# Kernel tuning notes

Measured on AMD Instinct MI355X. Metric: run time of the kernel, lower is better.

## Reference

```python
import jax, jax.numpy as jnp
import numpy as np

M, OUT, IN = 16384, 2048, 2048

def setup_inputs() -> dict:
    key = jax.random.key(0)
    k1, k2 = jax.random.split(key)
    x = jax.random.normal(k1, (M, IN), dtype=jnp.float32)
    weight = jax.random.normal(k2, (OUT, IN), dtype=jnp.float32)  # nn.Linear weight [out, in]
    alpha = jnp.ones((1,), dtype=jnp.float32) * 0.5
    return {"x": x, "weight": weight, "alpha": alpha}

def reference(x, weight, alpha):
    # DualRateAlphaFunction forward: binarize weight to sign(w) and scale by learned alpha.
    binary_weight = jnp.sign(weight) * alpha  # [out, in]
    # F.linear(x, binary_weight): x @ binary_weight.T
    return jnp.einsum('mi,oi->mo', x, binary_weight)
```

## Files before the change

### kernel.cpp

```cpp
#include <hip/hip_runtime.h>
#include <stdint.h>
#include <type_traits>

#define M_DIM 16384
#define N_DIM 2048
#define K_DIM 2048

typedef __bf16 bf16_t;
typedef __bf16 bf16x8 __attribute__((ext_vector_type(8)));
typedef __bf16 bf16x4 __attribute__((ext_vector_type(4)));
typedef float f32x4 __attribute__((ext_vector_type(4)));
typedef float f32x16 __attribute__((ext_vector_type(16)));

template <int N> using ic = std::integral_constant<int, N>;

__device__ __forceinline__ void gload_lds16(const void* g, void* l) {
  __builtin_amdgcn_global_load_lds(
      (const __attribute__((address_space(1))) void*)g,
      (__attribute__((address_space(3))) void*)l, 16, 0, 0);
}

template <bool SIGN>
__global__ void cvt_kernel(const float* __restrict__ in, bf16_t* __restrict__ out) {
  long long i = ((long long)blockIdx.x * 256 + threadIdx.x) * 8;
  const float4* p = (const float4*)(in + i);
  float4 v0 = p[0];
  float4 v1 = p[1];
  float f[8] = {v0.x, v0.y, v0.z, v0.w, v1.x, v1.y, v1.z, v1.w};
  bf16x8 r;
#pragma unroll
  for (int j = 0; j < 8; ++j) {
    float v = f[j];
    if (SIGN) v = (v > 0.f) ? 1.f : ((v < 0.f) ? -1.f : 0.f);
    r[j] = (bf16_t)v;
  }
  *(bf16x8*)(out + i) = r;
}

__global__ __launch_bounds__(512, 2) void gemm32(const bf16_t* __restrict__ A,
                                                 const bf16_t* __restrict__ B,
                                                 const float* __restrict__ alpha_p,
                                                 float* __restrict__ C) {
  extern __shared__ char smem[];
  char* AsB = smem;
  char* BsB = smem + 65536;

  const int tid = threadIdx.x;
  const int lane = tid & 63;
  const int wid = tid >> 6;
  const int wm = wid >> 2;
  const int wn = wid & 3;

  const int bid = blockIdx.x;
  const int swz = (bid & 7) * 64 + (bid >> 3);
  const int bm = swz >> 3;
  const int bn = swz & 7;

  const int rl = lane & 31;
  const int kh = lane >> 5;

  const char* apc[4][2];
  const char* bpc[2][2];
#pragma unroll
  for (int mt = 0; mt < 4; ++mt)
#pragma unroll
    for (int k2 = 0; k2 < 2; ++k2) {
      int row = wm * 128 + mt * 32 + rl;
      int c2 = k2 * 32 + kh * 16;
      apc[mt][k2] = AsB + row * 64 + (c2 ^ (((row >> 1) & 3) << 4));
    }
#pragma unroll
  for (int nt = 0; nt < 2; ++nt)
#pragma unroll
    for (int k2 = 0; k2 < 2; ++k2) {
      int row = wn * 64 + nt * 32 + rl;
      int c2 = k2 * 32 + kh * 16;
      bpc[nt][k2] = BsB + row * 64 + (c2 ^ (((row >> 1) & 3) << 4));
    }

  const char* asrc[2];
  const char* bsrc[2];
  char* aldst[2];
  char* bldst[2];
#pragma unroll
  for (int q = 0; q < 2; ++q) {
    int P = q * 8192 + tid * 16;
    int row = P >> 6;
    int lcol = (P & 63) ^ (((row >> 1) & 3) << 4);
    asrc[q] = (const char*)(A + (size_t)(bm * 256 + row) * K_DIM) + lcol;
    bsrc[q] = (const char*)(B + (size_t)(bn * 256 + row) * K_DIM) + lcol;
    aldst[q] = AsB + q * 8192 + wid * 1024;
    bldst[q] = BsB + q * 8192 + wid * 1024;
  }

  f32x16 acc[4][2];
#pragma unroll
  for (int mt = 0; mt < 4; ++mt)
#pragma unroll
    for (int nt = 0; nt < 2; ++nt)
#pragma unroll
      for (int r = 0; r < 16; ++r) acc[mt][nt][r] = 0.f;

#pragma unroll
  for (int tt = 0; tt < 3; ++tt) {
    gload_lds16(asrc[0] + tt * 64, aldst[0] + tt * 16384);
    gload_lds16(asrc[1] + tt * 64, aldst[1] + tt * 16384);
    gload_lds16(bsrc[0] + tt * 64, bldst[0] + tt * 16384);
    gload_lds16(bsrc[1] + tt * 64, bldst[1] + tt * 16384);
  }
  asm volatile("s_waitcnt vmcnt(8)" ::: "memory");
  __builtin_amdgcn_s_barrier();

  auto kstep = [&](auto UC, auto MC) {
    constexpr int U = UC.value;
    constexpr int MODE = MC.value;
    constexpr int SLOT = U * 16384;
    constexpr int PSLOT = ((U + 3) & 3) * 16384;
    constexpr int GOFF = (U + 3) * 64;

    bf16x8 a01[2][2], b[2][2];
#pragma unroll
    for (int mt = 0; mt < 2; ++mt)
#pragma unroll
      for (int k2 = 0; k2 < 2; ++k2)
        a01[mt][k2] = *(const bf16x8*)(apc[mt][k2] + SLOT);
#pragma unroll
    for (int nt = 0; nt < 2; ++nt)
#pragma unroll
      for (int k2 = 0; k2 < 2; ++k2)
        b[nt][k2] = *(const bf16x8*)(bpc[nt][k2] + SLOT);
    if constexpr (MODE == 0) {
      gload_lds16(asrc[0] + GOFF, aldst[0] + PSLOT);
      gload_lds16(asrc[1] + GOFF, aldst[1] + PSLOT);
    }
    __builtin_amdgcn_s_barrier();
    asm volatile("s_waitcnt lgkmcnt(0)" ::: "memory");
    __builtin_amdgcn_s_setprio(1);
#pragma unroll
    for (int k2 = 0; k2 < 2; ++k2)
#pragma unroll
      for (int mt = 0; mt < 2; ++mt)
#pragma unroll
        for (int nt = 0; nt < 2; ++nt)
          acc[mt][nt] = __builtin_amdgcn_mfma_f32_32x32x16_bf16(
              a01[mt][k2], b[nt][k2], acc[mt][nt], 0, 0, 0);
    __builtin_amdgcn_s_setprio(0);
    __builtin_amdgcn_s_barrier();

    bf16x8 a23[2][2];
#pragma unroll
    for (int mt = 0; mt < 2; ++mt)
#pragma unroll
      for (int k2 = 0; k2 < 2; ++k2)
        a23[mt][k2] = *(const bf16x8*)(apc[2 + mt][k2] + SLOT);
    if constexpr (MODE == 0) {
      gload_lds16(bsrc[0] + GOFF, bldst[0] + PSLOT);
      gload_lds16(bsrc[1] + GOFF, bldst[1] + PSLOT);
      asm volatile("s_waitcnt vmcnt(8)" ::: "memory");
    } else if constexpr (MODE == 1) {
      asm volatile("s_waitcnt vmcnt(4)" ::: "memory");
    } else {
      asm volatile("s_waitcnt vmcnt(0)" ::: "memory");
    }
    __builtin_amdgcn_s_barrier();
    asm volatile("s_waitcnt lgkmcnt(0)" ::: "memory");
    __builtin_amdgcn_s_setprio(1);
#pragma unroll
    for (int k2 = 0; k2 < 2; ++k2)
#pragma unroll
      for (int mt = 0; mt < 2; ++mt)
#pragma unroll
        for (int nt = 0; nt < 2; ++nt)
          acc[2 + mt][nt] = __builtin_amdgcn_mfma_f32_32x32x16_bf16(
              a23[mt][k2], b[nt][k2], acc[2 + mt][nt], 0, 0, 0);
    __builtin_amdgcn_s_setprio(0);
    __builtin_amdgcn_s_barrier();
  };

#pragma unroll 1
  for (int T = 0; T < 15; ++T) {
    kstep(ic<0>{}, ic<0>{});
    kstep(ic<1>{}, ic<0>{});
    kstep(ic<2>{}, ic<0>{});
    kstep(ic<3>{}, ic<0>{});
    asrc[0] += 256; asrc[1] += 256; bsrc[0] += 256; bsrc[1] += 256;
  }
  kstep(ic<0>{}, ic<0>{});
  kstep(ic<1>{}, ic<1>{});
  kstep(ic<2>{}, ic<2>{});
  kstep(ic<3>{}, ic<2>{});

  const float alpha = alpha_p[0];
  const int rbase = bm * 256 + wm * 128;
  const int cbase = bn * 256 + wn * 64 + rl;
#pragma unroll
  for (int mt = 0; mt < 4; ++mt)
#pragma unroll
    for (int nt = 0; nt < 2; ++nt)
#pragma unroll
      for (int r = 0; r < 16; ++r) {
        int rr = (r & 3) + 8 * (r >> 2) + 4 * kh;
        C[(size_t)(rbase + mt * 32 + rr) * N_DIM + cbase + nt * 32] =
            alpha * acc[mt][nt][r];
      }
}

__global__ __launch_bounds__(256) void gemm_fallback(const float* __restrict__ Ap,
                                                     const float* __restrict__ Bp,
                                                     const float* __restrict__ alpha_p,
                                                     float* __restrict__ C) {
  __shared__ bf16_t Asf[128 * 32];
  __shared__ bf16_t Bsf[128 * 32];
  const int tid = threadIdx.x;
  const int lane = tid & 63;
  const int wid = tid >> 6;
  const int wr = wid >> 1;
  const int wc = wid & 1;
  const int cpx = gridDim.x >> 3;
  const int bid = blockIdx.x;
  const int swz = (bid & 7) * cpx + (bid >> 3);
  const int NB = N_DIM / 128;
  const int bm = swz / NB;
  const int bn = swz % NB;
  f32x4 acc[4][4];
#pragma unroll
  for (int m = 0; m < 4; ++m)
#pragma unroll
    for (int n = 0; n < 4; ++n) acc[m][n] = (f32x4){0.f, 0.f, 0.f, 0.f};
  const int r0 = lane & 15;
  const int ko = (lane >> 4) * 8;
  for (int kk = 0; kk < K_DIM; kk += 32) {
    const float* Af = Ap + (size_t)bm * 128 * K_DIM + kk;
    const float* Bf = Bp + (size_t)bn * 128 * K_DIM + kk;
#pragma unroll
    for (int q = 0; q < 4; ++q) {
      int e = q * 256 + tid;
      int row = e >> 3;
      int kc = (e & 7) << 2;
      float4 v = *(const float4*)(Af + (size_t)row * K_DIM + kc);
      bf16x4 tv;
      tv[0] = (bf16_t)v.x; tv[1] = (bf16_t)v.y; tv[2] = (bf16_t)v.z; tv[3] = (bf16_t)v.w;
      *(bf16x4*)&Asf[e * 4] = tv;
    }
#pragma unroll
    for (int q = 0; q < 4; ++q) {
      int e = q * 256 + tid;
      int row = e >> 3;
      int kc = (e & 7) << 2;
      float4 v = *(const float4*)(Bf + (size_t)row * K_DIM + kc);
      float s[4] = {v.x, v.y, v.z, v.w};
      bf16x4 tv;
#pragma unroll
      for (int j = 0; j < 4; ++j)
        tv[j] = (bf16_t)((s[j] > 0.f) ? 1.f : ((s[j] < 0.f) ? -1.f : 0.f));
      *(bf16x4*)&Bsf[e * 4] = tv;
    }
    __syncthreads();
    bf16x8 a[4], b[4];
#pragma unroll
    for (int m = 0; m < 4; ++m) a[m] = *(const bf16x8*)&Asf[(wr * 64 + m * 16 + r0) * 32 + ko];
#pragma unroll
    for (int n = 0; n < 4; ++n) b[n] = *(const bf16x8*)&Bsf[(wc * 64 + n * 16 + r0) * 32 + ko];
#pragma unroll
    for (int m = 0; m < 4; ++m)
#pragma unroll
      for (int n = 0; n < 4; ++n)
        acc[m][n] = __builtin_amdgcn_mfma_f32_16x16x32_bf16(a[m], b[n], acc[m][n], 0, 0, 0);
    __syncthreads();
  }
  const float alpha = alpha_p[0];
  const int rowb = bm * 128 + wr * 64 + (lane >> 4) * 4;
  const int colb = bn * 128 + wc * 64 + r0;
#pragma unroll
  for (int m = 0; m < 4; ++m)
#pragma unroll
    for (int n = 0; n < 4; ++n)
#pragma unroll
      for (int r = 0; r < 4; ++r)
        C[(size_t)(rowb + m * 16 + r) * N_DIM + colb + n * 16] = alpha * acc[m][n][r];
}

extern "C" void kernel_launch(void* const* d_in, const int* in_sizes, int n_in,
                              void* d_out, int out_size, void* d_ws, size_t ws_size,
                              hipStream_t stream) {
  const float* x = (const float*)d_in[0];
  const float* w = (const float*)d_in[1];
  const float* alpha = (const float*)d_in[2];
  float* out = (float*)d_out;

  const size_t nx = (size_t)M_DIM * K_DIM;
  const size_t nw = (size_t)N_DIM * K_DIM;
  const size_t need = (nx + nw) * sizeof(bf16_t);

  if (ws_size >= need) {
    bf16_t* xb = (bf16_t*)d_ws;
    bf16_t* wb = xb + nx;
    cvt_kernel<false><<<(int)(nx / 2048), 256, 0, stream>>>(x, xb);
    cvt_kernel<true><<<(int)(nw / 2048), 256, 0, stream>>>(w, wb);
    (void)hipFuncSetAttribute((const void*)gemm32,
                              hipFuncAttributeMaxDynamicSharedMemorySize, 131072);
    gemm32<<<512, 512, 131072, stream>>>(xb, wb, alpha, out);
  } else {
    gemm_fallback<<<(M_DIM / 128) * (N_DIM / 128), 256, 0, stream>>>(x, w, alpha, out);
  }
}
```

Measured before the change: 172.3 us.

## Prefetch next-slot LDS fragments across k-steps and re-layout LDS in 16-row subblocks

Restructures the GEMM main loop so the A01 and B fragments for the next k-slot are read from LDS during the current step, using double-buffered B registers. This removes one barrier and an lgkmcnt(0) wait per half-step and issues all four global-to-LDS prefetches together. It also changes the LDS tile layout to 16-row subblocks with a new XOR swizzle, aiming to cut bank conflicts on the fragment reads. In exchange it holds more VGPRs for the register double-buffering and adds a MODE 3 path for the final step.

```diff
diff --git a/kernel.cpp b/kernel.cpp
--- a/kernel.cpp
+++ b/kernel.cpp
@@ -61,22 +61,21 @@
 
   const char* apc[4][2];
   const char* bpc[2][2];
-#pragma unroll
-  for (int mt = 0; mt < 4; ++mt)
-#pragma unroll
-    for (int k2 = 0; k2 < 2; ++k2) {
-      int row = wm * 128 + mt * 32 + rl;
-      int c2 = k2 * 32 + kh * 16;
-      apc[mt][k2] = AsB + row * 64 + (c2 ^ (((row >> 1) & 3) << 4));
-    }
-#pragma unroll
-  for (int nt = 0; nt < 2; ++nt)
-#pragma unroll
-    for (int k2 = 0; k2 < 2; ++k2) {
-      int row = wn * 64 + nt * 32 + rl;
-      int c2 = k2 * 32 + kh * 16;
-      bpc[nt][k2] = BsB + row * 64 + (c2 ^ (((row >> 1) & 3) << 4));
-    }
+  {
+    const int r15 = rl & 15;
+    const int rhi = rl >> 4;
+    const int swc = ((rhi << 5) | (kh << 4)) ^ (((r15 >> 1) & 3) << 4);
+#pragma unroll
+    for (int mt = 0; mt < 4; ++mt)
+#pragma unroll
+      for (int k2 = 0; k2 < 2; ++k2)
+        apc[mt][k2] = AsB + (wm * 4 + mt) * 2048 + k2 * 1024 + r15 * 64 + swc;
+#pragma unroll
+    for (int nt = 0; nt < 2; ++nt)
+#pragma unroll
+      for (int k2 = 0; k2 < 2; ++k2)
+        bpc[nt][k2] = BsB + (wn * 2 + nt) * 2048 + k2 * 1024 + r15 * 64 + swc;
+  }
 
   const char* asrc[2];
   const char* bsrc[2];
@@ -85,10 +84,18 @@
 #pragma unroll
   for (int q = 0; q < 2; ++q) {
     int P = q * 8192 + tid * 16;
-    int row = P >> 6;
-    int lcol = (P & 63) ^ (((row >> 1) & 3) << 4);
-    asrc[q] = (const char*)(A + (size_t)(bm * 256 + row) * K_DIM) + lcol;
-    bsrc[q] = (const char*)(B + (size_t)(bn * 256 + row) * K_DIM) + lcol;
+    int sb = P >> 11;
+    int p11 = P & 2047;
+    int k2 = p11 >> 10;
+    int r15 = (p11 >> 6) & 15;
+    int c = p11 & 63;
+    int un = c ^ (((r15 >> 1) & 3) << 4);
+    int rhi = un >> 5;
+    int khh = (un >> 4) & 1;
+    int row = sb * 32 + rhi * 16 + r15;
+    int kb = k2 * 32 + khh * 16;
+    asrc[q] = (const char*)A + (size_t)(bm * 256 + row) * (K_DIM * 2) + kb;
+    bsrc[q] = (const char*)B + (size_t)(bn * 256 + row) * (K_DIM * 2) + kb;
     aldst[q] = AsB + q * 8192 + wid * 1024;
     bldst[q] = BsB + q * 8192 + wid * 1024;
   }
@@ -100,6 +107,8 @@
     for (int nt = 0; nt < 2; ++nt)
 #pragma unroll
       for (int r = 0; r < 16; ++r) acc[mt][nt][r] = 0.f;
+
+  bf16x8 a01[2][2], a23[2][2], bfr[2][2][2];
 
 #pragma unroll
   for (int tt = 0; tt < 3; ++tt) {
@@ -110,31 +119,37 @@
   }
   asm volatile("s_waitcnt vmcnt(8)" ::: "memory");
   __builtin_amdgcn_s_barrier();
+#pragma unroll
+  for (int mt = 0; mt < 2; ++mt)
+#pragma unroll
+    for (int k2 = 0; k2 < 2; ++k2)
+      a01[mt][k2] = *(const bf16x8*)(apc[mt][k2]);
+#pragma unroll
+  for (int nt = 0; nt < 2; ++nt)
+#pragma unroll
+    for (int k2 = 0; k2 < 2; ++k2)
+      bfr[0][nt][k2] = *(const bf16x8*)(bpc[nt][k2]);
 
   auto kstep = [&](auto UC, auto MC) {
     constexpr int U = UC.value;
     constexpr int MODE = MC.value;
     constexpr int SLOT = U * 16384;
+    constexpr int NSLOT = ((U + 1) & 3) * 16384;
     constexpr int PSLOT = ((U + 3) & 3) * 16384;
     constexpr int GOFF = (U + 3) * 64;
-
-    bf16x8 a01[2][2], b[2][2];
+    constexpr int PAR = U & 1;
+
 #pragma unroll
     for (int mt = 0; mt < 2; ++mt)
 #pragma unroll
       for (int k2 = 0; k2 < 2; ++k2)
-        a01[mt][k2] = *(const bf16x8*)(apc[mt][k2] + SLOT);
-#pragma unroll
-    for (int nt = 0; nt < 2; ++nt)
-#pragma unroll
-      for (int k2 = 0; k2 < 2; ++k2)
-        b[nt][k2] = *(const bf16x8*)(bpc[nt][k2] + SLOT);
+        a23[mt][k2] = *(const bf16x8*)(apc[2 + mt][k2] + SLOT);
     if constexpr (MODE == 0) {
       gload_lds16(asrc[0] + GOFF, aldst[0] + PSLOT);
       gload_lds16(asrc[1] + GOFF, aldst[1] + PSLOT);
-    }
-    __builtin_amdgcn_s_barrier();
-    asm volatile("s_waitcnt lgkmcnt(0)" ::: "memory");
+      gload_lds16(bsrc[0] + GOFF, bldst[0] + PSLOT);
+      gload_lds16(bsrc[1] + GOFF, bldst[1] + PSLOT);
+    }
     __builtin_amdgcn_s_setprio(1);
 #pragma unroll
     for (int k2 = 0; k2 < 2; ++k2)
@@ -143,27 +158,29 @@
 #pragma unroll
         for (int nt = 0; nt < 2; ++nt)
           acc[mt][nt] = __builtin_amdgcn_mfma_f32_32x32x16_bf16(
-              a01[mt][k2], b[nt][k2], acc[mt][nt], 0, 0, 0);
+              a01[mt][k2], bfr[PAR][nt][k2], acc[mt][nt], 0, 0, 0);
     __builtin_amdgcn_s_setprio(0);
-    __builtin_amdgcn_s_barrier();
-
-    bf16x8 a23[2][2];
-#pragma unroll
-    for (int mt = 0; mt < 2; ++mt)
-#pragma unroll
-      for (int k2 = 0; k2 < 2; ++k2)
-        a23[mt][k2] = *(const bf16x8*)(apc[2 + mt][k2] + SLOT);
     if constexpr (MODE == 0) {
-      gload_lds16(bsrc[0] + GOFF, bldst[0] + PSLOT);
-      gload_lds16(bsrc[1] + GOFF, bldst[1] + PSLOT);
       asm volatile("s_waitcnt vmcnt(8)" ::: "memory");
     } else if constexpr (MODE == 1) {
       asm volatile("s_waitcnt vmcnt(4)" ::: "memory");
-    } else {
+    } else if constexpr (MODE == 2) {
       asm volatile("s_waitcnt vmcnt(0)" ::: "memory");
     }
     __builtin_amdgcn_s_barrier();
-    asm volatile("s_waitcnt lgkmcnt(0)" ::: "memory");
+
+    if constexpr (MODE != 3) {
+#pragma unroll
+      for (int mt = 0; mt < 2; ++mt)
+#pragma unroll
+        for (int k2 = 0; k2 < 2; ++k2)
+          a01[mt][k2] = *(const bf16x8*)(apc[mt][k2] + NSLOT);
+#pragma unroll
+      for (int nt = 0; nt < 2; ++nt)
+#pragma unroll
+        for (int k2 = 0; k2 < 2; ++k2)
+          bfr[PAR ^ 1][nt][k2] = *(const bf16x8*)(bpc[nt][k2] + NSLOT);
+    }
     __builtin_amdgcn_s_setprio(1);
 #pragma unroll
     for (int k2 = 0; k2 < 2; ++k2)
@@ -172,7 +189,7 @@
 #pragma unroll
         for (int nt = 0; nt < 2; ++nt)
           acc[2 + mt][nt] = __builtin_amdgcn_mfma_f32_32x32x16_bf16(
-              a23[mt][k2], b[nt][k2], acc[2 + mt][nt], 0, 0, 0);
+              a23[mt][k2], bfr[PAR][nt][k2], acc[2 + mt][nt], 0, 0, 0);
     __builtin_amdgcn_s_setprio(0);
     __builtin_amdgcn_s_barrier();
   };
@@ -188,7 +205,7 @@
   kstep(ic<0>{}, ic<0>{});
   kstep(ic<1>{}, ic<1>{});
   kstep(ic<2>{}, ic<2>{});
-  kstep(ic<3>{}, ic<2>{});
+  kstep(ic<3>{}, ic<3>{});
 
   const float alpha = alpha_p[0];
   const int rbase = bm * 256 + wm * 128;
```

Result: no change. 171.6 us (-0.4%).

## Restructure GEMM to 16x16x32 MFMA with K=64 double-buffered tiles and 8-phase schedule

Applied to the files above, without the earlier changes.

Replaces the 32x32x16 MFMA main loop with 16x16x32 bf16 MFMAs. The LDS layout changes from four K=32 stages to two K=64 stages with a new XOR swizzle. Each k-step is split into four MFMA phases that reuse A and B fragments (bL/bH halves), and the next tile's global-to-LDS loads are issued inside the same buffer after its reads complete. The goal is better MFMA issue density, fewer barriers per K element, and larger loads. The trade-offs are shallower prefetch depth (two buffers instead of four) and a riskier in-place refill ordering.

```diff
diff --git a/kernel.cpp b/kernel.cpp
--- a/kernel.cpp
+++ b/kernel.cpp
@@ -10,7 +10,6 @@
 typedef __bf16 bf16x8 __attribute__((ext_vector_type(8)));
 typedef __bf16 bf16x4 __attribute__((ext_vector_type(4)));
 typedef float f32x4 __attribute__((ext_vector_type(4)));
-typedef float f32x16 __attribute__((ext_vector_type(16)));
 
 template <int N> using ic = std::integral_constant<int, N>;
 
@@ -37,13 +36,11 @@
   *(bf16x8*)(out + i) = r;
 }
 
-__global__ __launch_bounds__(512, 2) void gemm32(const bf16_t* __restrict__ A,
+__global__ __launch_bounds__(512, 2) void gemm8p(const bf16_t* __restrict__ A,
                                                  const bf16_t* __restrict__ B,
                                                  const float* __restrict__ alpha_p,
                                                  float* __restrict__ C) {
   extern __shared__ char smem[];
-  char* AsB = smem;
-  char* BsB = smem + 65536;
 
   const int tid = threadIdx.x;
   const int lane = tid & 63;
@@ -56,57 +53,46 @@
   const int bm = swz >> 3;
   const int bn = swz & 7;
 
-  const int rl = lane & 31;
-  const int kh = lane >> 5;
-
-  const char* apc[4][2];
-  const char* bpc[2][2];
-#pragma unroll
-  for (int mt = 0; mt < 4; ++mt)
-#pragma unroll
-    for (int k2 = 0; k2 < 2; ++k2) {
-      int row = wm * 128 + mt * 32 + rl;
-      int c2 = k2 * 32 + kh * 16;
-      apc[mt][k2] = AsB + row * 64 + (c2 ^ (((row >> 1) & 3) << 4));
-    }
-#pragma unroll
-  for (int nt = 0; nt < 2; ++nt)
-#pragma unroll
-    for (int k2 = 0; k2 < 2; ++k2) {
-      int row = wn * 64 + nt * 32 + rl;
-      int c2 = k2 * 32 + kh * 16;
-      bpc[nt][k2] = BsB + row * 64 + (c2 ^ (((row >> 1) & 3) << 4));
-    }
-
-  const char* asrc[2];
-  const char* bsrc[2];
-  char* aldst[2];
-  char* bldst[2];
-#pragma unroll
-  for (int q = 0; q < 2; ++q) {
-    int P = q * 8192 + tid * 16;
-    int row = P >> 6;
-    int lcol = (P & 63) ^ (((row >> 1) & 3) << 4);
-    asrc[q] = (const char*)(A + (size_t)(bm * 256 + row) * K_DIM) + lcol;
-    bsrc[q] = (const char*)(B + (size_t)(bn * 256 + row) * K_DIM) + lcol;
-    aldst[q] = AsB + q * 8192 + wid * 1024;
-    bldst[q] = BsB + q * 8192 + wid * 1024;
-  }
-
-  f32x16 acc[4][2];
-#pragma unroll
-  for (int mt = 0; mt < 4; ++mt)
-#pragma unroll
-    for (int nt = 0; nt < 2; ++nt)
-#pragma unroll
-      for (int r = 0; r < 16; ++r) acc[mt][nt][r] = 0.f;
-
-#pragma unroll
-  for (int tt = 0; tt < 3; ++tt) {
-    gload_lds16(asrc[0] + tt * 64, aldst[0] + tt * 16384);
-    gload_lds16(asrc[1] + tt * 64, aldst[1] + tt * 16384);
-    gload_lds16(bsrc[0] + tt * 64, bldst[0] + tt * 16384);
-    gload_lds16(bsrc[1] + tt * 64, bldst[1] + tt * 16384);
+  const int q = lane >> 4;
+  const int r15 = lane & 15;
+
+  const int swc = (r15 & 7) << 4;
+  int aoff[2], boff[2];
+#pragma unroll
+  for (int k = 0; k < 2; ++k) {
+    int ck = (k * 64 + q * 16) ^ swc;
+    aoff[k] = (wm * 128 + r15) * 128 + ck;
+    boff[k] = 32768 + (wn * 64 + r15) * 128 + ck;
+  }
+
+  const char* asrc[4];
+  const char* bsrc[4];
+  int adsto[4], bdsto[4];
+#pragma unroll
+  for (int j = 0; j < 4; ++j) {
+    int P = j * 8192 + tid * 16;
+    int row = P >> 7;
+    int lcol = (P & 127) ^ ((row & 7) << 4);
+    asrc[j] = (const char*)A + (size_t)(bm * 256 + row) * (K_DIM * 2) + lcol;
+    bsrc[j] = (const char*)B + (size_t)(bn * 256 + row) * (K_DIM * 2) + lcol;
+    adsto[j] = j * 8192 + wid * 1024;
+    bdsto[j] = 32768 + j * 8192 + wid * 1024;
+  }
+
+  f32x4 acc[8][4];
+#pragma unroll
+  for (int mt = 0; mt < 8; ++mt)
+#pragma unroll
+    for (int nt = 0; nt < 4; ++nt) acc[mt][nt] = (f32x4){0.f, 0.f, 0.f, 0.f};
+
+#pragma unroll
+  for (int t = 0; t < 2; ++t) {
+#pragma unroll
+    for (int j = 0; j < 4; ++j)
+      gload_lds16(asrc[j] + t * 128, smem + t * 65536 + adsto[j]);
+#pragma unroll
+    for (int j = 0; j < 4; ++j)
+      gload_lds16(bsrc[j] + t * 128, smem + t * 65536 + bdsto[j]);
   }
   asm volatile("s_waitcnt vmcnt(8)" ::: "memory");
   __builtin_amdgcn_s_barrier();
@@ -114,65 +100,96 @@
   auto kstep = [&](auto UC, auto MC) {
     constexpr int U = UC.value;
     constexpr int MODE = MC.value;
-    constexpr int SLOT = U * 16384;
-    constexpr int PSLOT = ((U + 3) & 3) * 16384;
-    constexpr int GOFF = (U + 3) * 64;
-
-    bf16x8 a01[2][2], b[2][2];
-#pragma unroll
-    for (int mt = 0; mt < 2; ++mt)
-#pragma unroll
-      for (int k2 = 0; k2 < 2; ++k2)
-        a01[mt][k2] = *(const bf16x8*)(apc[mt][k2] + SLOT);
+    constexpr int TB = U * 65536;
+    constexpr int GOFF = (U + 2) * 128;
+
+    bf16x8 a[4][2], bL[2][2], bH[2][2];
+
+#pragma unroll
+    for (int mt = 0; mt < 4; ++mt)
+#pragma unroll
+      for (int k = 0; k < 2; ++k)
+        a[mt][k] = *(const bf16x8*)(smem + TB + aoff[k] + mt * 2048);
 #pragma unroll
     for (int nt = 0; nt < 2; ++nt)
 #pragma unroll
-      for (int k2 = 0; k2 < 2; ++k2)
-        b[nt][k2] = *(const bf16x8*)(bpc[nt][k2] + SLOT);
-    if constexpr (MODE == 0) {
-      gload_lds16(asrc[0] + GOFF, aldst[0] + PSLOT);
-      gload_lds16(asrc[1] + GOFF, aldst[1] + PSLOT);
-    }
+      for (int k = 0; k < 2; ++k)
+        bL[nt][k] = *(const bf16x8*)(smem + TB + boff[k] + nt * 2048);
     __builtin_amdgcn_s_barrier();
     asm volatile("s_waitcnt lgkmcnt(0)" ::: "memory");
     __builtin_amdgcn_s_setprio(1);
 #pragma unroll
-    for (int k2 = 0; k2 < 2; ++k2)
-#pragma unroll
-      for (int mt = 0; mt < 2; ++mt)
+    for (int k = 0; k < 2; ++k)
+#pragma unroll
+      for (int mt = 0; mt < 4; ++mt)
 #pragma unroll
         for (int nt = 0; nt < 2; ++nt)
-          acc[mt][nt] = __builtin_amdgcn_mfma_f32_32x32x16_bf16(
-              a01[mt][k2], b[nt][k2], acc[mt][nt], 0, 0, 0);
+          acc[mt][nt] = __builtin_amdgcn_mfma_f32_16x16x32_bf16(
+              a[mt][k], bL[nt][k], acc[mt][nt], 0, 0, 0);
     __builtin_amdgcn_s_setprio(0);
     __builtin_amdgcn_s_barrier();
 
-    bf16x8 a23[2][2];
-#pragma unroll
-    for (int mt = 0; mt < 2; ++mt)
-#pragma unroll
-      for (int k2 = 0; k2 < 2; ++k2)
-        a23[mt][k2] = *(const bf16x8*)(apc[2 + mt][k2] + SLOT);
+#pragma unroll
+    for (int nt = 0; nt < 2; ++nt)
+#pragma unroll
+      for (int k = 0; k < 2; ++k)
+        bH[nt][k] = *(const bf16x8*)(smem + TB + boff[k] + (2 + nt) * 2048);
+    __builtin_amdgcn_s_barrier();
+    asm volatile("s_waitcnt lgkmcnt(0)" ::: "memory");
+    __builtin_amdgcn_s_setprio(1);
+#pragma unroll
+    for (int k = 0; k < 2; ++k)
+#pragma unroll
+      for (int mt = 0; mt < 4; ++mt)
+#pragma unroll
+        for (int nt = 0; nt < 2; ++nt)
+          acc[mt][2 + nt] = __builtin_amdgcn_mfma_f32_16x16x32_bf16(
+              a[mt][k], bH[nt][k], acc[mt][2 + nt], 0, 0, 0);
+    __builtin_amdgcn_s_setprio(0);
+    __builtin_amdgcn_s_barrier();
+
+#pragma unroll
+    for (int mt = 0; mt < 4; ++mt)
+#pragma unroll
+      for (int k = 0; k < 2; ++k)
+        a[mt][k] = *(const bf16x8*)(smem + TB + aoff[k] + (4 + mt) * 2048);
     if constexpr (MODE == 0) {
-      gload_lds16(bsrc[0] + GOFF, bldst[0] + PSLOT);
-      gload_lds16(bsrc[1] + GOFF, bldst[1] + PSLOT);
+#pragma unroll
+      for (int j = 0; j < 4; ++j)
+        gload_lds16(bsrc[j] + GOFF, smem + TB + bdsto[j]);
+    }
+    __builtin_amdgcn_s_barrier();
+    asm volatile("s_waitcnt lgkmcnt(0)" ::: "memory");
+    __builtin_amdgcn_s_setprio(1);
+#pragma unroll
+    for (int k = 0; k < 2; ++k)
+#pragma unroll
+      for (int mt = 0; mt < 4; ++mt)
+#pragma unroll
+        for (int nt = 0; nt < 2; ++nt)
+          acc[4 + mt][2 + nt] = __builtin_amdgcn_mfma_f32_16x16x32_bf16(
+              a[mt][k], bH[nt][k], acc[4 + mt][2 + nt], 0, 0, 0);
+    __builtin_amdgcn_s_setprio(0);
+    __builtin_amdgcn_s_barrier();
+
+    if constexpr (MODE == 0) {
+#pragma unroll
+      for (int j = 0; j < 4; ++j)
+        gload_lds16(asrc[j] + GOFF, smem + TB + adsto[j]);
       asm volatile("s_waitcnt vmcnt(8)" ::: "memory");
     } else if constexpr (MODE == 1) {
-      asm volatile("s_waitcnt vmcnt(4)" ::: "memory");
-    } else {
       asm volatile("s_waitcnt vmcnt(0)" ::: "memory");
     }
     __builtin_amdgcn_s_barrier();
-    asm volatile("s_waitcnt lgkmcnt(0)" ::: "memory");
     __builtin_amdgcn_s_setprio(1);
 #pragma unroll
-    for (int k2 = 0; k2 < 2; ++k2)
-#pragma unroll
-      for (int mt = 0; mt < 2; ++mt)
+    for (int k = 0; k < 2; ++k)
+#pragma unroll
+      for (int mt = 0; mt < 4; ++mt)
 #pragma unroll
         for (int nt = 0; nt < 2; ++nt)
-          acc[2 + mt][nt] = __builtin_amdgcn_mfma_f32_32x32x16_bf16(
-              a23[mt][k2], b[nt][k2], acc[2 + mt][nt], 0, 0, 0);
+          acc[4 + mt][nt] = __builtin_amdgcn_mfma_f32_16x16x32_bf16(
+              a[mt][k], bL[nt][k], acc[4 + mt][nt], 0, 0, 0);
     __builtin_amdgcn_s_setprio(0);
     __builtin_amdgcn_s_barrier();
   };
@@ -181,28 +198,23 @@
   for (int T = 0; T < 15; ++T) {
     kstep(ic<0>{}, ic<0>{});
     kstep(ic<1>{}, ic<0>{});
-    kstep(ic<2>{}, ic<0>{});
-    kstep(ic<3>{}, ic<0>{});
-    asrc[0] += 256; asrc[1] += 256; bsrc[0] += 256; bsrc[1] += 256;
-  }
-  kstep(ic<0>{}, ic<0>{});
-  kstep(ic<1>{}, ic<1>{});
-  kstep(ic<2>{}, ic<2>{});
-  kstep(ic<3>{}, ic<2>{});
+#pragma unroll
+    for (int j = 0; j < 4; ++j) { asrc[j] += 256; bsrc[j] += 256; }
+  }
+  kstep(ic<0>{}, ic<1>{});
+  kstep(ic<1>{}, ic<2>{});
 
   const float alpha = alpha_p[0];
-  const int rbase = bm * 256 + wm * 128;
-  const int cbase = bn * 256 + wn * 64 + rl;
-#pragma unroll
-  for (int mt = 0; mt < 4; ++mt)
-#pragma unroll
-    for (int nt = 0; nt < 2; ++nt)
-#pragma unroll
-      for (int r = 0; r < 16; ++r) {
-        int rr = (r & 3) + 8 * (r >> 2) + 4 * kh;
-        C[(size_t)(rbase + mt * 32 + rr) * N_DIM + cbase + nt * 32] =
+  const int rbase = bm * 256 + wm * 128 + q * 4;
+  const int cbase = bn * 256 + wn * 64 + r15;
+#pragma unroll
+  for (int mt = 0; mt < 8; ++mt)
+#pragma unroll
+    for (int nt = 0; nt < 4; ++nt)
+#pragma unroll
+      for (int r = 0; r < 4; ++r)
+        C[(size_t)(rbase + mt * 16 + r) * N_DIM + cbase + nt * 16] =
             alpha * acc[mt][nt][r];
-      }
 }
 
 __global__ __launch_bounds__(256) void gemm_fallback(const float* __restrict__ Ap,
@@ -233,8 +245,8 @@
     const float* Af = Ap + (size_t)bm * 128 * K_DIM + kk;
     const float* Bf = Bp + (size_t)bn * 128 * K_DIM + kk;
 #pragma unroll
-    for (int q = 0; q < 4; ++q) {
-      int e = q * 256 + tid;
+    for (int qq = 0; qq < 4; ++qq) {
+      int e = qq * 256 + tid;
       int row = e >> 3;
       int kc = (e & 7) << 2;
       float4 v = *(const float4*)(Af + (size_t)row * K_DIM + kc);
@@ -243,8 +255,8 @@
       *(bf16x4*)&Asf[e * 4] = tv;
     }
 #pragma unroll
-    for (int q = 0; q < 4; ++q) {
-      int e = q * 256 + tid;
+    for (int qq = 0; qq < 4; ++qq) {
+      int e = qq * 256 + tid;
       int row = e >> 3;
       int kc = (e & 7) << 2;
       float4 v = *(const float4*)(Bf + (size_t)row * K_DIM + kc);
@@ -297,9 +309,9 @@
     bf16_t* wb = xb + nx;
     cvt_kernel<false><<<(int)(nx / 2048), 256, 0, stream>>>(x, xb);
     cvt_kernel<true><<<(int)(nw / 2048), 256, 0, stream>>>(w, wb);
-    (void)hipFuncSetAttribute((const void*)gemm32,
+    (void)hipFuncSetAttribute((const void*)gemm8p,
                               hipFuncAttributeMaxDynamicSharedMemorySize, 131072);
-    gemm32<<<512, 512, 131072, stream>>>(xb, wb, alpha, out);
+    gemm8p<<<512, 512, 131072, stream>>>(xb, wb, alpha, out);
   } else {
     gemm_fallback<<<(M_DIM / 128) * (N_DIM / 128), 256, 0, stream>>>(x, w, alpha, out);
   }
```

New measurement: 168.5 us. -2.2%, faster.
